# Kernel optimization log

Measured on AMD Instinct MI355X. Metric: run time of the kernel, lower is better.

The kernel has to match this reference:

```python
import jax, jax.numpy as jnp
import numpy as np

IN = 128      # input_size
HID = 64      # fast_net hidden width
NFW = IN * HID + HID  # 8256 flat fast weights (layer1 then layer2)
B = 256


def setup_inputs() -> dict:
    key = jax.random.key(0)
    k1, k2, k3, k4 = jax.random.split(key, 4)
    x = jax.random.normal(k1, (B, 1, IN), dtype=jnp.float32)
    # updater network weights: Linear(IN, 2*NFW, bias=False) then Linear(2*NFW, NFW, bias=False)
    W1 = jax.random.normal(k2, (2 * NFW, IN), dtype=jnp.float32) * 0.02
    W2 = jax.random.normal(k3, (NFW, 2 * NFW), dtype=jnp.float32) * 0.02
    # initial flat fast weights, in (0,1) since the update squashes there
    fw0 = jax.random.uniform(k4, (NFW,), dtype=jnp.float32)
    return {"x": x, "W1": W1, "W2": W2, "fw0": fw0}


def reference(x, W1, W2, fw0):
    xs = x[:, 0, :]  # [B, IN]
    # updater network has no weight updates itself -> batch the two matmuls
    U = (xs @ W1.T) @ W2.T  # [B, NFW] per-sample weight updates
    gain, shift = jnp.float32(10.0), jnp.float32(0.5)

    def step(fw, inp):
        x_i, u_i = inp
        # update_func: 1 / (1 + exp(-10*(w + u - 0.5)))
        fw = jax.nn.sigmoid(gain * (fw + u_i - shift))
        w1 = fw[: IN * HID].reshape(HID, IN)   # fast layer 1 [HID, IN]
        w2 = fw[IN * HID:].reshape(1, HID)     # fast layer 2 [1, HID]
        pred = w2 @ jax.nn.relu(w1 @ x_i)      # [1]
        return fw, pred

    _, preds = jax.lax.scan(step, fw0, (xs, U))  # sequential over batch, state persists
    return preds  # [B, 1]
```

## Files before the change

### kernel.cpp

```cpp
#include <hip/hip_runtime.h>
#include <hip/hip_bf16.h>

#define IN_DIM 128
#define HID    64
#define NFW    8256
#define BATCH  256
#define K2     16512
#define BM     64
#define NMB    129
#define KSPLIT 6
#define NT_PER 43
#define GRID_M 774

typedef float f32x4 __attribute__((ext_vector_type(4)));
typedef short bf16x8 __attribute__((ext_vector_type(8)));

__device__ __forceinline__ unsigned int f2bf(float f) {
    union { float f; unsigned int u; } v; v.f = f;
    return (v.u + 0x7FFFu + ((v.u >> 16) & 1u)) >> 16;
}

__device__ __forceinline__ bf16x8 pack8(f32x4 a, f32x4 b) {
    union { bf16x8 v; __hip_bfloat162 h[4]; } u;
    u.h[0] = __float22bfloat162_rn(float2{a.x, a.y});
    u.h[1] = __float22bfloat162_rn(float2{a.z, a.w});
    u.h[2] = __float22bfloat162_rn(float2{b.x, b.y});
    u.h[3] = __float22bfloat162_rn(float2{b.z, b.w});
    return u.v;
}

#define GLL16(SRC, DST)                                                        \
    __builtin_amdgcn_global_load_lds(                                          \
        (const __attribute__((address_space(1))) unsigned int*)(SRC),          \
        (__attribute__((address_space(3))) unsigned int*)(DST), 16, 0, 0)

__global__ __launch_bounds__(256) void k_prep_w1t(const float* __restrict__ W1,
                                                  unsigned short* __restrict__ W1T) {
    __shared__ float tile[64][IN_DIM + 1];
    const int kt = blockIdx.x;
    const int t  = threadIdx.x;
    const float* src = W1 + (size_t)kt * 64 * IN_DIM;
#pragma unroll
    for (int p = 0; p < 8; ++p) {
        int c4 = p * 256 + t;
        int e = c4 * 4;
        int row = e >> 7, col = e & 127;
        f32x4 v = *reinterpret_cast<const f32x4*>(src + row * IN_DIM + col);
        tile[row][col+0] = v.x; tile[row][col+1] = v.y;
        tile[row][col+2] = v.z; tile[row][col+3] = v.w;
    }
    __syncthreads();
    unsigned short* dst = W1T + (size_t)kt * (IN_DIM * 64);
#pragma unroll
    for (int it = 0; it < 4; ++it) {
        int c = it * 256 + t;
        int n = c >> 3, kl0 = (c & 7) * 8;
        uint4 w;
        w.x = f2bf(tile[kl0+0][n]) | (f2bf(tile[kl0+1][n]) << 16);
        w.y = f2bf(tile[kl0+2][n]) | (f2bf(tile[kl0+3][n]) << 16);
        w.z = f2bf(tile[kl0+4][n]) | (f2bf(tile[kl0+5][n]) << 16);
        w.w = f2bf(tile[kl0+6][n]) | (f2bf(tile[kl0+7][n]) << 16);
        *reinterpret_cast<uint4*>(dst + c * 8) = w;
    }
}

__global__ __launch_bounds__(256) void k_gemm_M(const float* __restrict__ W2,
                                                const unsigned short* __restrict__ W1T,
                                                float* __restrict__ Mpart) {
    __shared__ __align__(16) unsigned char smem[65536];
    float* trs = reinterpret_cast<float*>(smem);

    const int t = threadIdx.x;
    const int lane = t & 63, wid = t >> 6;
    const int wm = wid >> 1, wn = wid & 1;
    const int l15 = lane & 15, l4 = (lane >> 4) & 3;

    const int b = blockIdx.x;
    const int xcd = b & 7, slot = b >> 3;
    const int p = (xcd < 6) ? (xcd * 97 + slot) : (582 + (xcd - 6) * 96 + slot);
    const int ks = p / NMB, mb = p % NMB;

    const int m0 = mb * BM;
    const int g0 = ks * NT_PER;
    const int kt0 = (p * 7) % NT_PER;

    const int ca0 = wid * 4;
    const int rl0 = 4 * (ca0 + 0) + (lane >> 4);
    const int rl1 = 4 * (ca0 + 1) + (lane >> 4);
    const int rl2 = 4 * (ca0 + 2) + (lane >> 4);
    const int rl3 = 4 * (ca0 + 3) + (lane >> 4);
    const int acb = (lane & 15) * 16;
    const float* aS0 = W2 + (size_t)(m0 + rl0) * K2 + (size_t)g0 * 64 + ((acb ^ ((rl0 & 7) << 4)) >> 2);
    const float* aS1 = W2 + (size_t)(m0 + rl1) * K2 + (size_t)g0 * 64 + ((acb ^ ((rl1 & 7) << 4)) >> 2);
    const float* aS2 = W2 + (size_t)(m0 + rl2) * K2 + (size_t)g0 * 64 + ((acb ^ ((rl2 & 7) << 4)) >> 2);
    const float* aS3 = W2 + (size_t)(m0 + rl3) * K2 + (size_t)g0 * 64 + ((acb ^ ((rl3 & 7) << 4)) >> 2);
    const int rb0 = 8 * (ca0 + 0) + (lane >> 3);
    const int rb1 = 8 * (ca0 + 1) + (lane >> 3);
    const int rb2 = 8 * (ca0 + 2) + (lane >> 3);
    const int rb3 = 8 * (ca0 + 3) + (lane >> 3);
    const int bcb = (lane & 7) * 16;
    const unsigned short* bS0 = W1T + (size_t)g0 * 8192 + rb0 * 64 + ((bcb ^ ((rb0 & 7) << 4)) >> 1);
    const unsigned short* bS1 = W1T + (size_t)g0 * 8192 + rb1 * 64 + ((bcb ^ ((rb1 & 7) << 4)) >> 1);
    const unsigned short* bS2 = W1T + (size_t)g0 * 8192 + rb2 * 64 + ((bcb ^ ((rb2 & 7) << 4)) >> 1);
    const unsigned short* bS3 = W1T + (size_t)g0 * 8192 + rb3 * 64 + ((bcb ^ ((rb3 & 7) << 4)) >> 1);
    const int aD = ca0 * 1024;

    f32x4 acc[2][4];
#pragma unroll
    for (int mf = 0; mf < 2; ++mf)
#pragma unroll
        for (int nf = 0; nf < 4; ++nf)
            acc[mf][nf] = (f32x4){0.f, 0.f, 0.f, 0.f};

#define ISSUE_AB(BUF, KT) {                                                    \
    unsigned char* _ab = smem + (BUF) * 16384;                                 \
    unsigned char* _bb = smem + 32768 + (BUF) * 16384;                         \
    const size_t _ao = (size_t)(KT) * 64;                                      \
    const size_t _bo = (size_t)(KT) * 8192;                                    \
    GLL16(aS0 + _ao, _ab + aD);                                                \
    GLL16(aS1 + _ao, _ab + aD + 1024);                                         \
    GLL16(aS2 + _ao, _ab + aD + 2048);                                         \
    GLL16(aS3 + _ao, _ab + aD + 3072);                                         \
    GLL16(bS0 + _bo, _bb + aD);                                                \
    GLL16(bS1 + _bo, _bb + aD + 1024);                                         \
    GLL16(bS2 + _bo, _bb + aD + 2048);                                         \
    GLL16(bS3 + _bo, _bb + aD + 3072);                                         \
}

#define MFMA_PHASE(BUF) {                                                      \
    const unsigned char* _Ash = smem + (BUF) * 16384;                          \
    const unsigned char* _Bsh = smem + 32768 + (BUF) * 16384;                  \
    _Pragma("unroll")                                                          \
    for (int kk = 0; kk < 2; ++kk) {                                           \
        const int _ar0 = wm * 32 + l15;                                        \
        const int _ar1 = wm * 32 + 16 + l15;                                   \
        const int _pb  = kk * 128 + l4 * 32;                                   \
        const int _s0  = (_ar0 & 7) << 4;                                      \
        const int _s1  = (_ar1 & 7) << 4;                                      \
        f32x4 _x0 = *reinterpret_cast<const f32x4*>(&_Ash[_ar0 * 256 + ((_pb)      ^ _s0)]); \
        f32x4 _x1 = *reinterpret_cast<const f32x4*>(&_Ash[_ar0 * 256 + ((_pb + 16) ^ _s0)]); \
        f32x4 _y0 = *reinterpret_cast<const f32x4*>(&_Ash[_ar1 * 256 + ((_pb)      ^ _s1)]); \
        f32x4 _y1 = *reinterpret_cast<const f32x4*>(&_Ash[_ar1 * 256 + ((_pb + 16) ^ _s1)]); \
        bf16x8 af0 = pack8(_x0, _x1);                                          \
        bf16x8 af1 = pack8(_y0, _y1);                                          \
        const int _fsw = (l15 & 7) << 4;                                       \
        const int _fc  = (kk * 64 + l4 * 16) ^ _fsw;                           \
        bf16x8 bf0 = *reinterpret_cast<const bf16x8*>(&_Bsh[(wn * 64 +  0 + l15) * 128 + _fc]); \
        bf16x8 bf1 = *reinterpret_cast<const bf16x8*>(&_Bsh[(wn * 64 + 16 + l15) * 128 + _fc]); \
        bf16x8 bf2 = *reinterpret_cast<const bf16x8*>(&_Bsh[(wn * 64 + 32 + l15) * 128 + _fc]); \
        bf16x8 bf3 = *reinterpret_cast<const bf16x8*>(&_Bsh[(wn * 64 + 48 + l15) * 128 + _fc]); \
        acc[0][0] = __builtin_amdgcn_mfma_f32_16x16x32_bf16(af0, bf0, acc[0][0], 0, 0, 0); \
        acc[0][1] = __builtin_amdgcn_mfma_f32_16x16x32_bf16(af0, bf1, acc[0][1], 0, 0, 0); \
        acc[0][2] = __builtin_amdgcn_mfma_f32_16x16x32_bf16(af0, bf2, acc[0][2], 0, 0, 0); \
        acc[0][3] = __builtin_amdgcn_mfma_f32_16x16x32_bf16(af0, bf3, acc[0][3], 0, 0, 0); \
        acc[1][0] = __builtin_amdgcn_mfma_f32_16x16x32_bf16(af1, bf0, acc[1][0], 0, 0, 0); \
        acc[1][1] = __builtin_amdgcn_mfma_f32_16x16x32_bf16(af1, bf1, acc[1][1], 0, 0, 0); \
        acc[1][2] = __builtin_amdgcn_mfma_f32_16x16x32_bf16(af1, bf2, acc[1][2], 0, 0, 0); \
        acc[1][3] = __builtin_amdgcn_mfma_f32_16x16x32_bf16(af1, bf3, acc[1][3], 0, 0, 0); \
    } }

    int tcur = kt0;
    ISSUE_AB(0, tcur);
    __syncthreads();

    int cur = 0;
#pragma unroll 1
    for (int i = 0; i < NT_PER; ++i) {
        if (i + 1 < NT_PER) {
            int tn = tcur + 1; if (tn >= NT_PER) tn = 0;
            ISSUE_AB(cur ^ 1, tn);
            tcur = tn;
        }
        MFMA_PHASE(cur);
        __syncthreads();
        cur ^= 1;
    }

    float* outp = Mpart + (size_t)ks * ((size_t)NFW * IN_DIM) + (size_t)m0 * IN_DIM;
#pragma unroll 1
    for (int w = 0; w < 2; ++w) {
        __syncthreads();
        if (wm == w) {
#pragma unroll
            for (int mf = 0; mf < 2; ++mf)
#pragma unroll
                for (int nf = 0; nf < 4; ++nf)
#pragma unroll
                    for (int r = 0; r < 4; ++r)
                        trs[(mf * 16 + l4 * 4 + r) * 132 + wn * 64 + nf * 16 + l15] = acc[mf][nf][r];
        }
        __syncthreads();
#pragma unroll
        for (int q = 0; q < 4; ++q) {
            int idx = q * 256 + t;
            int rr = idx >> 5, c4 = (idx & 31) << 2;
            f32x4 v = *reinterpret_cast<const f32x4*>(&trs[rr * 132 + c4]);
            *reinterpret_cast<f32x4*>(outp + (size_t)(w * 32 + rr) * IN_DIM + c4) = v;
        }
    }
#undef ISSUE_AB
#undef MFMA_PHASE
}

__global__ __launch_bounds__(256) void k_reduce_M(const float* __restrict__ Mpart,
                                                  unsigned short* __restrict__ Mb) {
    const int idx = blockIdx.x * 256 + threadIdx.x;
    f32x4 s = (f32x4){0.f, 0.f, 0.f, 0.f};
#pragma unroll
    for (int ks = 0; ks < KSPLIT; ++ks) {
        f32x4 v = *reinterpret_cast<const f32x4*>(
            Mpart + (size_t)ks * ((size_t)NFW * IN_DIM) + (size_t)idx * 4);
        s.x += v.x; s.y += v.y; s.z += v.z; s.w += v.w;
    }
    uint2 o;
    o.x = f2bf(s.x) | (f2bf(s.y) << 16);
    o.y = f2bf(s.z) | (f2bf(s.w) << 16);
    *reinterpret_cast<uint2*>(Mb + (size_t)idx * 4) = o;
}

__global__ __launch_bounds__(256) void k_uchains(const float* __restrict__ xs,
                                                 const unsigned short* __restrict__ Mb,
                                                 const float* __restrict__ fw0,
                                                 float* __restrict__ FW) {
    __shared__ float Ulds[256][68];
    const int t = threadIdx.x, lane = t & 63, wid = t >> 6;
    const int l15 = lane & 15, l4 = (lane >> 4) & 3;
    const int j0 = blockIdx.x * 64;

    bf16x8 bfr[4][4];
#pragma unroll
    for (int kk = 0; kk < 4; ++kk)
#pragma unroll
        for (int nf = 0; nf < 4; ++nf)
            bfr[kk][nf] = *reinterpret_cast<const bf16x8*>(
                Mb + (size_t)(j0 + nf * 16 + l15) * IN_DIM + kk * 32 + l4 * 8);

#pragma unroll 1
    for (int ib = 0; ib < 4; ++ib) {
        const int i0 = wid * 64 + ib * 16;
        f32x4 acc[4];
#pragma unroll
        for (int nf = 0; nf < 4; ++nf) acc[nf] = (f32x4){0.f, 0.f, 0.f, 0.f};
#pragma unroll
        for (int kk = 0; kk < 4; ++kk) {
            const float* xp = xs + (size_t)(i0 + l15) * IN_DIM + kk * 32 + l4 * 8;
            f32x4 x0 = *reinterpret_cast<const f32x4*>(xp);
            f32x4 x1 = *reinterpret_cast<const f32x4*>(xp + 4);
            union { bf16x8 v; unsigned short s[8]; } af;
            af.s[0] = f2bf(x0.x); af.s[1] = f2bf(x0.y);
            af.s[2] = f2bf(x0.z); af.s[3] = f2bf(x0.w);
            af.s[4] = f2bf(x1.x); af.s[5] = f2bf(x1.y);
            af.s[6] = f2bf(x1.z); af.s[7] = f2bf(x1.w);
#pragma unroll
            for (int nf = 0; nf < 4; ++nf)
                acc[nf] = __builtin_amdgcn_mfma_f32_16x16x32_bf16(af.v, bfr[kk][nf], acc[nf], 0, 0, 0);
        }
#pragma unroll
        for (int nf = 0; nf < 4; ++nf)
#pragma unroll
            for (int r = 0; r < 4; ++r)
                Ulds[i0 + l4 * 4 + r][nf * 16 + l15] = acc[nf][r];
    }
    __syncthreads();

    if (wid == 0) {
        const int j = j0 + lane;
        float fw = fw0[j];
        float* fp = FW + j;
#pragma unroll 8
        for (int i = 0; i < BATCH; ++i) {
            float u = Ulds[i][lane];
            float z = 10.0f * (fw + u - 0.5f);
            fw = 1.0f / (1.0f + __expf(-z));
            fp[(size_t)i * NFW] = fw;
        }
    }
}

__global__ __launch_bounds__(256) void k_preds(const float* __restrict__ FW,
                                               const float* __restrict__ xs,
                                               float* __restrict__ out) {
    __shared__ float xsh[IN_DIM];
    __shared__ float hsh[HID];
    const int i = blockIdx.x, t = threadIdx.x;
    if (t < 32) {
        f32x4 v = *reinterpret_cast<const f32x4*>(xs + (size_t)i * IN_DIM + t * 4);
        xsh[t*4+0] = v.x; xsh[t*4+1] = v.y; xsh[t*4+2] = v.z; xsh[t*4+3] = v.w;
    }
    __syncthreads();
    const int k = t >> 2, q = t & 3;
    const float* fr = FW + (size_t)i * NFW + k * IN_DIM + q * 32;
    float p = 0.f;
#pragma unroll
    for (int m = 0; m < 8; ++m) {
        f32x4 v = *reinterpret_cast<const f32x4*>(fr + m * 4);
        const int d = q * 32 + m * 4;
        p += v.x * xsh[d] + v.y * xsh[d+1] + v.z * xsh[d+2] + v.w * xsh[d+3];
    }
    p += __shfl_xor(p, 1);
    p += __shfl_xor(p, 2);
    if (q == 0) hsh[k] = fmaxf(p, 0.f);
    __syncthreads();
    if (t < 64) {
        float v = FW[(size_t)i * NFW + IN_DIM * HID + t] * hsh[t];
        v += __shfl_xor(v, 1);  v += __shfl_xor(v, 2);  v += __shfl_xor(v, 4);
        v += __shfl_xor(v, 8);  v += __shfl_xor(v, 16); v += __shfl_xor(v, 32);
        if (t == 0) out[i] = v;
    }
}

extern "C" void kernel_launch(void* const* d_in, const int* in_sizes, int n_in,
                              void* d_out, int out_size, void* d_ws, size_t ws_size,
                              hipStream_t stream) {
    const float* x   = (const float*)d_in[0];
    const float* W1  = (const float*)d_in[1];
    const float* W2  = (const float*)d_in[2];
    const float* fw0 = (const float*)d_in[3];
    float* out = (float*)d_out;

    char* ws = (char*)d_ws;
    unsigned short* W1T   = (unsigned short*)(ws);
    float*          Mpart = (float*)(ws + 4227072);
    unsigned short* Mb    = (unsigned short*)(ws + 29589504);
    float*          FW    = (float*)(ws + 31703040);

    hipLaunchKernelGGL(k_prep_w1t, dim3(258),    dim3(256), 0, stream, W1, W1T);
    hipLaunchKernelGGL(k_gemm_M,   dim3(GRID_M), dim3(256), 0, stream, W2, W1T, Mpart);
    hipLaunchKernelGGL(k_reduce_M, dim3(1032),   dim3(256), 0, stream, Mpart, Mb);
    hipLaunchKernelGGL(k_uchains,  dim3(129),    dim3(256), 0, stream, x, Mb, fw0, FW);
    hipLaunchKernelGGL(k_preds,    dim3(256),    dim3(256), 0, stream, FW, x, out);
}
```

Before: 165.5 us.

## Enlarge GEMM M-tile to 96 rows and fuse split-K reduction into uchains

The W2·W1 GEMM now uses 96-row tiles (three MFMA row fragments per wave), which cuts the grid from 774 to 516 blocks so each block does more work per B-tile load. The remap of blocks across XCDs is adjusted to match. The separate k_reduce_M kernel is removed, and k_uchains sums the six split-K partials directly while loading its fragments, saving one launch and the intermediate bf16 write and read. In exchange, LDS use rises to 80KB and register pressure grows, which may lower occupancy. The chain kernel also makes redundant strided fp32 reads across only 129 blocks.

```diff
diff --git a/kernel.cpp b/kernel.cpp
--- a/kernel.cpp
+++ b/kernel.cpp
@@ -6,11 +6,11 @@
 #define NFW    8256
 #define BATCH  256
 #define K2     16512
-#define BM     64
-#define NMB    129
+#define BM     96
+#define NMB    86
 #define KSPLIT 6
 #define NT_PER 43
-#define GRID_M 774
+#define GRID_M 516
 
 typedef float f32x4 __attribute__((ext_vector_type(4)));
 typedef short bf16x8 __attribute__((ext_vector_type(8)));
@@ -67,7 +67,7 @@
 __global__ __launch_bounds__(256) void k_gemm_M(const float* __restrict__ W2,
                                                 const unsigned short* __restrict__ W1T,
                                                 float* __restrict__ Mpart) {
-    __shared__ __align__(16) unsigned char smem[65536];
+    __shared__ __align__(16) unsigned char smem[81920];
     float* trs = reinterpret_cast<float*>(smem);
 
     const int t = threadIdx.x;
@@ -77,74 +77,84 @@
 
     const int b = blockIdx.x;
     const int xcd = b & 7, slot = b >> 3;
-    const int p = (xcd < 6) ? (xcd * 97 + slot) : (582 + (xcd - 6) * 96 + slot);
+    const int p = (xcd < 4) ? (xcd * 65 + slot) : (260 + (xcd - 4) * 64 + slot);
     const int ks = p / NMB, mb = p % NMB;
 
     const int m0 = mb * BM;
     const int g0 = ks * NT_PER;
     const int kt0 = (p * 7) % NT_PER;
 
-    const int ca0 = wid * 4;
-    const int rl0 = 4 * (ca0 + 0) + (lane >> 4);
-    const int rl1 = 4 * (ca0 + 1) + (lane >> 4);
-    const int rl2 = 4 * (ca0 + 2) + (lane >> 4);
-    const int rl3 = 4 * (ca0 + 3) + (lane >> 4);
+    const int caA = wid * 6;
     const int acb = (lane & 15) * 16;
+    const int rl0 = 4 * (caA + 0) + (lane >> 4);
+    const int rl1 = 4 * (caA + 1) + (lane >> 4);
+    const int rl2 = 4 * (caA + 2) + (lane >> 4);
+    const int rl3 = 4 * (caA + 3) + (lane >> 4);
+    const int rl4 = 4 * (caA + 4) + (lane >> 4);
+    const int rl5 = 4 * (caA + 5) + (lane >> 4);
     const float* aS0 = W2 + (size_t)(m0 + rl0) * K2 + (size_t)g0 * 64 + ((acb ^ ((rl0 & 7) << 4)) >> 2);
     const float* aS1 = W2 + (size_t)(m0 + rl1) * K2 + (size_t)g0 * 64 + ((acb ^ ((rl1 & 7) << 4)) >> 2);
     const float* aS2 = W2 + (size_t)(m0 + rl2) * K2 + (size_t)g0 * 64 + ((acb ^ ((rl2 & 7) << 4)) >> 2);
     const float* aS3 = W2 + (size_t)(m0 + rl3) * K2 + (size_t)g0 * 64 + ((acb ^ ((rl3 & 7) << 4)) >> 2);
-    const int rb0 = 8 * (ca0 + 0) + (lane >> 3);
-    const int rb1 = 8 * (ca0 + 1) + (lane >> 3);
-    const int rb2 = 8 * (ca0 + 2) + (lane >> 3);
-    const int rb3 = 8 * (ca0 + 3) + (lane >> 3);
+    const float* aS4 = W2 + (size_t)(m0 + rl4) * K2 + (size_t)g0 * 64 + ((acb ^ ((rl4 & 7) << 4)) >> 2);
+    const float* aS5 = W2 + (size_t)(m0 + rl5) * K2 + (size_t)g0 * 64 + ((acb ^ ((rl5 & 7) << 4)) >> 2);
+    const int caB = wid * 4;
     const int bcb = (lane & 7) * 16;
+    const int rb0 = 8 * (caB + 0) + (lane >> 3);
+    const int rb1 = 8 * (caB + 1) + (lane >> 3);
+    const int rb2 = 8 * (caB + 2) + (lane >> 3);
+    const int rb3 = 8 * (caB + 3) + (lane >> 3);
     const unsigned short* bS0 = W1T + (size_t)g0 * 8192 + rb0 * 64 + ((bcb ^ ((rb0 & 7) << 4)) >> 1);
     const unsigned short* bS1 = W1T + (size_t)g0 * 8192 + rb1 * 64 + ((bcb ^ ((rb1 & 7) << 4)) >> 1);
     const unsigned short* bS2 = W1T + (size_t)g0 * 8192 + rb2 * 64 + ((bcb ^ ((rb2 & 7) << 4)) >> 1);
     const unsigned short* bS3 = W1T + (size_t)g0 * 8192 + rb3 * 64 + ((bcb ^ ((rb3 & 7) << 4)) >> 1);
-    const int aD = ca0 * 1024;
-
-    f32x4 acc[2][4];
-#pragma unroll
-    for (int mf = 0; mf < 2; ++mf)
+    const int aD = caA * 1024;
+    const int bD = caB * 1024;
+
+    f32x4 acc[3][4];
+#pragma unroll
+    for (int mf = 0; mf < 3; ++mf)
 #pragma unroll
         for (int nf = 0; nf < 4; ++nf)
             acc[mf][nf] = (f32x4){0.f, 0.f, 0.f, 0.f};
 
 #define ISSUE_AB(BUF, KT) {                                                    \
-    unsigned char* _ab = smem + (BUF) * 16384;                                 \
-    unsigned char* _bb = smem + 32768 + (BUF) * 16384;                         \
+    unsigned char* _ab = smem + (BUF) * 24576;                                 \
+    unsigned char* _bb = smem + 49152 + (BUF) * 16384;                         \
     const size_t _ao = (size_t)(KT) * 64;                                      \
     const size_t _bo = (size_t)(KT) * 8192;                                    \
     GLL16(aS0 + _ao, _ab + aD);                                                \
     GLL16(aS1 + _ao, _ab + aD + 1024);                                         \
     GLL16(aS2 + _ao, _ab + aD + 2048);                                         \
     GLL16(aS3 + _ao, _ab + aD + 3072);                                         \
-    GLL16(bS0 + _bo, _bb + aD);                                                \
-    GLL16(bS1 + _bo, _bb + aD + 1024);                                         \
-    GLL16(bS2 + _bo, _bb + aD + 2048);                                         \
-    GLL16(bS3 + _bo, _bb + aD + 3072);                                         \
+    GLL16(aS4 + _ao, _ab + aD + 4096);                                         \
+    GLL16(aS5 + _ao, _ab + aD + 5120);                                         \
+    GLL16(bS0 + _bo, _bb + bD);                                                \
+    GLL16(bS1 + _bo, _bb + bD + 1024);                                         \
+    GLL16(bS2 + _bo, _bb + bD + 2048);                                         \
+    GLL16(bS3 + _bo, _bb + bD + 3072);                                         \
 }
 
 #define MFMA_PHASE(BUF) {                                                      \
-    const unsigned char* _Ash = smem + (BUF) * 16384;                          \
-    const unsigned char* _Bsh = smem + 32768 + (BUF) * 16384;                  \
+    const unsigned char* _Ash = smem + (BUF) * 24576;                          \
+    const unsigned char* _Bsh = smem + 49152 + (BUF) * 16384;                  \
+    const int _sw = (l15 & 7) << 4;                                            \
     _Pragma("unroll")                                                          \
     for (int kk = 0; kk < 2; ++kk) {                                           \
-        const int _ar0 = wm * 32 + l15;                                        \
-        const int _ar1 = wm * 32 + 16 + l15;                                   \
-        const int _pb  = kk * 128 + l4 * 32;                                   \
-        const int _s0  = (_ar0 & 7) << 4;                                      \
-        const int _s1  = (_ar1 & 7) << 4;                                      \
-        f32x4 _x0 = *reinterpret_cast<const f32x4*>(&_Ash[_ar0 * 256 + ((_pb)      ^ _s0)]); \
-        f32x4 _x1 = *reinterpret_cast<const f32x4*>(&_Ash[_ar0 * 256 + ((_pb + 16) ^ _s0)]); \
-        f32x4 _y0 = *reinterpret_cast<const f32x4*>(&_Ash[_ar1 * 256 + ((_pb)      ^ _s1)]); \
-        f32x4 _y1 = *reinterpret_cast<const f32x4*>(&_Ash[_ar1 * 256 + ((_pb + 16) ^ _s1)]); \
+        const int _pb = kk * 128 + l4 * 32;                                    \
+        const int _a0 = (wm * 48 +  0 + l15) * 256;                            \
+        const int _a1 = (wm * 48 + 16 + l15) * 256;                            \
+        const int _a2 = (wm * 48 + 32 + l15) * 256;                            \
+        f32x4 _x0 = *reinterpret_cast<const f32x4*>(&_Ash[_a0 + ((_pb)      ^ _sw)]); \
+        f32x4 _x1 = *reinterpret_cast<const f32x4*>(&_Ash[_a0 + ((_pb + 16) ^ _sw)]); \
+        f32x4 _y0 = *reinterpret_cast<const f32x4*>(&_Ash[_a1 + ((_pb)      ^ _sw)]); \
+        f32x4 _y1 = *reinterpret_cast<const f32x4*>(&_Ash[_a1 + ((_pb + 16) ^ _sw)]); \
+        f32x4 _z0 = *reinterpret_cast<const f32x4*>(&_Ash[_a2 + ((_pb)      ^ _sw)]); \
+        f32x4 _z1 = *reinterpret_cast<const f32x4*>(&_Ash[_a2 + ((_pb + 16) ^ _sw)]); \
         bf16x8 af0 = pack8(_x0, _x1);                                          \
         bf16x8 af1 = pack8(_y0, _y1);                                          \
-        const int _fsw = (l15 & 7) << 4;                                       \
-        const int _fc  = (kk * 64 + l4 * 16) ^ _fsw;                           \
+        bf16x8 af2 = pack8(_z0, _z1);                                          \
+        const int _fc = (kk * 64 + l4 * 16) ^ _sw;                             \
         bf16x8 bf0 = *reinterpret_cast<const bf16x8*>(&_Bsh[(wn * 64 +  0 + l15) * 128 + _fc]); \
         bf16x8 bf1 = *reinterpret_cast<const bf16x8*>(&_Bsh[(wn * 64 + 16 + l15) * 128 + _fc]); \
         bf16x8 bf2 = *reinterpret_cast<const bf16x8*>(&_Bsh[(wn * 64 + 32 + l15) * 128 + _fc]); \
@@ -157,6 +167,10 @@
         acc[1][1] = __builtin_amdgcn_mfma_f32_16x16x32_bf16(af1, bf1, acc[1][1], 0, 0, 0); \
         acc[1][2] = __builtin_amdgcn_mfma_f32_16x16x32_bf16(af1, bf2, acc[1][2], 0, 0, 0); \
         acc[1][3] = __builtin_amdgcn_mfma_f32_16x16x32_bf16(af1, bf3, acc[1][3], 0, 0, 0); \
+        acc[2][0] = __builtin_amdgcn_mfma_f32_16x16x32_bf16(af2, bf0, acc[2][0], 0, 0, 0); \
+        acc[2][1] = __builtin_amdgcn_mfma_f32_16x16x32_bf16(af2, bf1, acc[2][1], 0, 0, 0); \
+        acc[2][2] = __builtin_amdgcn_mfma_f32_16x16x32_bf16(af2, bf2, acc[2][2], 0, 0, 0); \
+        acc[2][3] = __builtin_amdgcn_mfma_f32_16x16x32_bf16(af2, bf3, acc[2][3], 0, 0, 0); \
     } }
 
     int tcur = kt0;
@@ -182,7 +196,7 @@
         __syncthreads();
         if (wm == w) {
 #pragma unroll
-            for (int mf = 0; mf < 2; ++mf)
+            for (int mf = 0; mf < 3; ++mf)
 #pragma unroll
                 for (int nf = 0; nf < 4; ++nf)
 #pragma unroll
@@ -191,35 +205,19 @@
         }
         __syncthreads();
 #pragma unroll
-        for (int q = 0; q < 4; ++q) {
+        for (int q = 0; q < 6; ++q) {
             int idx = q * 256 + t;
             int rr = idx >> 5, c4 = (idx & 31) << 2;
             f32x4 v = *reinterpret_cast<const f32x4*>(&trs[rr * 132 + c4]);
-            *reinterpret_cast<f32x4*>(outp + (size_t)(w * 32 + rr) * IN_DIM + c4) = v;
+            *reinterpret_cast<f32x4*>(outp + (size_t)(w * 48 + rr) * IN_DIM + c4) = v;
         }
     }
 #undef ISSUE_AB
 #undef MFMA_PHASE
 }
 
-__global__ __launch_bounds__(256) void k_reduce_M(const float* __restrict__ Mpart,
-                                                  unsigned short* __restrict__ Mb) {
-    const int idx = blockIdx.x * 256 + threadIdx.x;
-    f32x4 s = (f32x4){0.f, 0.f, 0.f, 0.f};
-#pragma unroll
-    for (int ks = 0; ks < KSPLIT; ++ks) {
-        f32x4 v = *reinterpret_cast<const f32x4*>(
-            Mpart + (size_t)ks * ((size_t)NFW * IN_DIM) + (size_t)idx * 4);
-        s.x += v.x; s.y += v.y; s.z += v.z; s.w += v.w;
-    }
-    uint2 o;
-    o.x = f2bf(s.x) | (f2bf(s.y) << 16);
-    o.y = f2bf(s.z) | (f2bf(s.w) << 16);
-    *reinterpret_cast<uint2*>(Mb + (size_t)idx * 4) = o;
-}
-
 __global__ __launch_bounds__(256) void k_uchains(const float* __restrict__ xs,
-                                                 const unsigned short* __restrict__ Mb,
+                                                 const float* __restrict__ Mpart,
                                                  const float* __restrict__ fw0,
                                                  float* __restrict__ FW) {
     __shared__ float Ulds[256][68];
@@ -231,9 +229,19 @@
 #pragma unroll
     for (int kk = 0; kk < 4; ++kk)
 #pragma unroll
-        for (int nf = 0; nf < 4; ++nf)
-            bfr[kk][nf] = *reinterpret_cast<const bf16x8*>(
-                Mb + (size_t)(j0 + nf * 16 + l15) * IN_DIM + kk * 32 + l4 * 8);
+        for (int nf = 0; nf < 4; ++nf) {
+            const int j = j0 + nf * 16 + l15;
+            f32x4 s0 = (f32x4){0.f, 0.f, 0.f, 0.f};
+            f32x4 s1 = (f32x4){0.f, 0.f, 0.f, 0.f};
+#pragma unroll
+            for (int ks = 0; ks < KSPLIT; ++ks) {
+                const float* mp = Mpart + (size_t)ks * ((size_t)NFW * IN_DIM)
+                                + (size_t)j * IN_DIM + kk * 32 + l4 * 8;
+                s0 += *reinterpret_cast<const f32x4*>(mp);
+                s1 += *reinterpret_cast<const f32x4*>(mp + 4);
+            }
+            bfr[kk][nf] = pack8(s0, s1);
+        }
 
 #pragma unroll 1
     for (int ib = 0; ib < 4; ++ib) {
@@ -246,14 +254,10 @@
             const float* xp = xs + (size_t)(i0 + l15) * IN_DIM + kk * 32 + l4 * 8;
             f32x4 x0 = *reinterpret_cast<const f32x4*>(xp);
             f32x4 x1 = *reinterpret_cast<const f32x4*>(xp + 4);
-            union { bf16x8 v; unsigned short s[8]; } af;
-            af.s[0] = f2bf(x0.x); af.s[1] = f2bf(x0.y);
-            af.s[2] = f2bf(x0.z); af.s[3] = f2bf(x0.w);
-            af.s[4] = f2bf(x1.x); af.s[5] = f2bf(x1.y);
-            af.s[6] = f2bf(x1.z); af.s[7] = f2bf(x1.w);
+            bf16x8 af = pack8(x0, x1);
 #pragma unroll
             for (int nf = 0; nf < 4; ++nf)
-                acc[nf] = __builtin_amdgcn_mfma_f32_16x16x32_bf16(af.v, bfr[kk][nf], acc[nf], 0, 0, 0);
+                acc[nf] = __builtin_amdgcn_mfma_f32_16x16x32_bf16(af, bfr[kk][nf], acc[nf], 0, 0, 0);
         }
 #pragma unroll
         for (int nf = 0; nf < 4; ++nf)
@@ -321,12 +325,10 @@
     char* ws = (char*)d_ws;
     unsigned short* W1T   = (unsigned short*)(ws);
     float*          Mpart = (float*)(ws + 4227072);
-    unsigned short* Mb    = (unsigned short*)(ws + 29589504);
-    float*          FW    = (float*)(ws + 31703040);
+    float*          FW    = (float*)(ws + 29589504);
 
     hipLaunchKernelGGL(k_prep_w1t, dim3(258),    dim3(256), 0, stream, W1, W1T);
     hipLaunchKernelGGL(k_gemm_M,   dim3(GRID_M), dim3(256), 0, stream, W2, W1T, Mpart);
-    hipLaunchKernelGGL(k_reduce_M, dim3(1032),   dim3(256), 0, stream, Mpart, Mb);
-    hipLaunchKernelGGL(k_uchains,  dim3(129),    dim3(256), 0, stream, x, Mb, fw0, FW);
+    hipLaunchKernelGGL(k_uchains,  dim3(129),    dim3(256), 0, stream, x, Mpart, fw0, FW);
     hipLaunchKernelGGL(k_preds,    dim3(256),    dim3(256), 0, stream, FW, x, out);
 }
```

Result: slower. 199.9 us (+20.8%).

## Cut K-split to four and fuse partial-sum reduction into U-chain kernel

Applied to the files above, without the earlier changes.

Reduces the split-K factor of the W2·W1 product GEMM from 6 to 4 (516 blocks, uneven 65/64 tile ranges) and removes the separate reduce kernel. The U-chain kernel now sums the fp32 partials itself while loading its B fragments and packs them to bf16. This drops one launch and the Mpart reread/Mb write pass, and shrinks partial-sum traffic, at the cost of fewer GEMM blocks (516 rather than 774), which may leave the GPU less fully occupied.

```diff
diff --git a/kernel.cpp b/kernel.cpp
--- a/kernel.cpp
+++ b/kernel.cpp
@@ -8,9 +8,8 @@
 #define K2     16512
 #define BM     64
 #define NMB    129
-#define KSPLIT 6
-#define NT_PER 43
-#define GRID_M 774
+#define KSPLIT 4
+#define GRID_M 516
 
 typedef float f32x4 __attribute__((ext_vector_type(4)));
 typedef short bf16x8 __attribute__((ext_vector_type(8)));
@@ -77,12 +76,13 @@
 
     const int b = blockIdx.x;
     const int xcd = b & 7, slot = b >> 3;
-    const int p = (xcd < 6) ? (xcd * 97 + slot) : (582 + (xcd - 6) * 96 + slot);
+    const int p = (xcd < 4) ? (xcd * 65 + slot) : (260 + (xcd - 4) * 64 + slot);
     const int ks = p / NMB, mb = p % NMB;
 
     const int m0 = mb * BM;
-    const int g0 = ks * NT_PER;
-    const int kt0 = (p * 7) % NT_PER;
+    const int NS = (ks < 2) ? 65 : 64;
+    const int g0 = ks * 64 + ((ks < 2) ? ks : 2);
+    const int kt0 = (p * 7) % NS;
 
     const int ca0 = wid * 4;
     const int rl0 = 4 * (ca0 + 0) + (lane >> 4);
@@ -165,9 +165,9 @@
 
     int cur = 0;
 #pragma unroll 1
-    for (int i = 0; i < NT_PER; ++i) {
-        if (i + 1 < NT_PER) {
-            int tn = tcur + 1; if (tn >= NT_PER) tn = 0;
+    for (int i = 0; i < NS; ++i) {
+        if (i + 1 < NS) {
+            int tn = tcur + 1; if (tn >= NS) tn = 0;
             ISSUE_AB(cur ^ 1, tn);
             tcur = tn;
         }
@@ -202,24 +202,8 @@
 #undef MFMA_PHASE
 }
 
-__global__ __launch_bounds__(256) void k_reduce_M(const float* __restrict__ Mpart,
-                                                  unsigned short* __restrict__ Mb) {
-    const int idx = blockIdx.x * 256 + threadIdx.x;
-    f32x4 s = (f32x4){0.f, 0.f, 0.f, 0.f};
-#pragma unroll
-    for (int ks = 0; ks < KSPLIT; ++ks) {
-        f32x4 v = *reinterpret_cast<const f32x4*>(
-            Mpart + (size_t)ks * ((size_t)NFW * IN_DIM) + (size_t)idx * 4);
-        s.x += v.x; s.y += v.y; s.z += v.z; s.w += v.w;
-    }
-    uint2 o;
-    o.x = f2bf(s.x) | (f2bf(s.y) << 16);
-    o.y = f2bf(s.z) | (f2bf(s.w) << 16);
-    *reinterpret_cast<uint2*>(Mb + (size_t)idx * 4) = o;
-}
-
 __global__ __launch_bounds__(256) void k_uchains(const float* __restrict__ xs,
-                                                 const unsigned short* __restrict__ Mb,
+                                                 const float* __restrict__ Mpart,
                                                  const float* __restrict__ fw0,
                                                  float* __restrict__ FW) {
     __shared__ float Ulds[256][68];
@@ -231,9 +215,19 @@
 #pragma unroll
     for (int kk = 0; kk < 4; ++kk)
 #pragma unroll
-        for (int nf = 0; nf < 4; ++nf)
-            bfr[kk][nf] = *reinterpret_cast<const bf16x8*>(
-                Mb + (size_t)(j0 + nf * 16 + l15) * IN_DIM + kk * 32 + l4 * 8);
+        for (int nf = 0; nf < 4; ++nf) {
+            const int j = j0 + nf * 16 + l15;
+            f32x4 s0 = (f32x4){0.f, 0.f, 0.f, 0.f};
+            f32x4 s1 = (f32x4){0.f, 0.f, 0.f, 0.f};
+#pragma unroll
+            for (int ks = 0; ks < KSPLIT; ++ks) {
+                const float* mp = Mpart + (size_t)ks * ((size_t)NFW * IN_DIM)
+                                + (size_t)j * IN_DIM + kk * 32 + l4 * 8;
+                s0 += *reinterpret_cast<const f32x4*>(mp);
+                s1 += *reinterpret_cast<const f32x4*>(mp + 4);
+            }
+            bfr[kk][nf] = pack8(s0, s1);
+        }
 
 #pragma unroll 1
     for (int ib = 0; ib < 4; ++ib) {
@@ -246,14 +240,10 @@
             const float* xp = xs + (size_t)(i0 + l15) * IN_DIM + kk * 32 + l4 * 8;
             f32x4 x0 = *reinterpret_cast<const f32x4*>(xp);
             f32x4 x1 = *reinterpret_cast<const f32x4*>(xp + 4);
-            union { bf16x8 v; unsigned short s[8]; } af;
-            af.s[0] = f2bf(x0.x); af.s[1] = f2bf(x0.y);
-            af.s[2] = f2bf(x0.z); af.s[3] = f2bf(x0.w);
-            af.s[4] = f2bf(x1.x); af.s[5] = f2bf(x1.y);
-            af.s[6] = f2bf(x1.z); af.s[7] = f2bf(x1.w);
+            bf16x8 af = pack8(x0, x1);
 #pragma unroll
             for (int nf = 0; nf < 4; ++nf)
-                acc[nf] = __builtin_amdgcn_mfma_f32_16x16x32_bf16(af.v, bfr[kk][nf], acc[nf], 0, 0, 0);
+                acc[nf] = __builtin_amdgcn_mfma_f32_16x16x32_bf16(af, bfr[kk][nf], acc[nf], 0, 0, 0);
         }
 #pragma unroll
         for (int nf = 0; nf < 4; ++nf)
@@ -321,12 +311,10 @@
     char* ws = (char*)d_ws;
     unsigned short* W1T   = (unsigned short*)(ws);
     float*          Mpart = (float*)(ws + 4227072);
-    unsigned short* Mb    = (unsigned short*)(ws + 29589504);
-    float*          FW    = (float*)(ws + 31703040);
+    float*          FW    = (float*)(ws + 21135360);
 
     hipLaunchKernelGGL(k_prep_w1t, dim3(258),    dim3(256), 0, stream, W1, W1T);
     hipLaunchKernelGGL(k_gemm_M,   dim3(GRID_M), dim3(256), 0, stream, W2, W1T, Mpart);
-    hipLaunchKernelGGL(k_reduce_M, dim3(1032),   dim3(256), 0, stream, Mpart, Mb);
-    hipLaunchKernelGGL(k_uchains,  dim3(129),    dim3(256), 0, stream, x, Mb, fw0, FW);
+    hipLaunchKernelGGL(k_uchains,  dim3(129),    dim3(256), 0, stream, x, Mpart, fw0, FW);
     hipLaunchKernelGGL(k_preds,    dim3(256),    dim3(256), 0, stream, FW, x, out);
 }
```

Measured after the change: 209.0 us. 1.26x slower.
